# Performance work log

Measured on AMD Instinct MI355X. Metric: run time of the kernel, lower is better.

Reference implementation:

```python
import jax, jax.numpy as jnp
import numpy as np

SCALE = 10.0
THRESH = 1e-3   # nn.Threshold(eps, 0)
NORM_EPS = 1e-12  # F.normalize default eps
LEAKY_SLOPE = 0.01


def _proj(x, W1, W2):
    # x: [B, C, L]; conv1x1 == channel matmul
    h = jnp.einsum('oc,bcl->bol', W1, x)
    h = jnp.where(h >= 0, h, LEAKY_SLOPE * h)
    return jnp.einsum('oc,bcl->bol', W2, h)


def _l2norm(x):
    # normalize over channel dim (dim=1), torch F.normalize semantics
    n = jnp.sqrt(jnp.sum(x * x, axis=1, keepdims=True))
    return x / jnp.maximum(n, NORM_EPS)


def setup_inputs() -> dict:
    key = jax.random.key(0)
    k1, k2, k3, k4 = jax.random.split(key, 4)
    B, C, L, OUT = 4, 64, 4096, 64
    query = jax.random.normal(k1, (B, C, L), dtype=jnp.float32)
    kv = jax.random.normal(k2, (B, C, L), dtype=jnp.float32)
    W1 = jax.random.normal(k3, (2 * C, C), dtype=jnp.float32) * (1.0 / np.sqrt(C))
    W2 = jax.random.normal(k4, (OUT, 2 * C), dtype=jnp.float32) * (1.0 / np.sqrt(2 * C))
    return {"query": query, "key": kv, "W1": W1, "W2": W2}


def reference(query, key, W1, W2):
    # self_attention=True: query_conv is key_conv (shared weights)
    q = _l2norm(_proj(query, W1, W2))   # [B, O, L]
    k = _l2norm(_proj(key, W1, W2))     # [B, O, L]
    scores = jnp.einsum('bcl,bcm->blm', q, k) * SCALE  # [B, L, L]
    w = jax.nn.softmax(scores, axis=-1)
    return jnp.where(w > THRESH, w, 0.0)
```

## Files before the change

kernel.cpp:

```cpp
#include <hip/hip_runtime.h>
#include <math.h>

#define B 4
#define C 64
#define L 4096
#define OUTC 64
#define SCALE 10.0f
#define THRESH 1e-3f

typedef float v2f __attribute__((ext_vector_type(2)));
typedef float v4f __attribute__((ext_vector_type(4)));

__device__ __forceinline__ v2f pk_fma(v2f a, v2f b, v2f c) {
#if __has_builtin(__builtin_elementwise_fma)
    return __builtin_elementwise_fma(a, b, c);
#else
    v2f r; r.x = fmaf(a.x, b.x, c.x); r.y = fmaf(a.y, b.y, c.y); return r;
#endif
}

__global__ void __launch_bounds__(256) proj_kernel(
    const float* __restrict__ q_in, const float* __restrict__ k_in,
    const float* __restrict__ W1, const float* __restrict__ W2,
    float* __restrict__ qp, float* __restrict__ kp)
{
    int bid   = blockIdx.x;
    int which = bid >> 8;
    int b     = (bid >> 6) & 3;
    int l0    = (bid & 63) << 6;
    int t     = threadIdx.x;
    int g     = t >> 6;
    int l     = t & 63;

    const float* __restrict__ src =
        (which ? k_in : q_in) + (size_t)b * C * L + l0 + l;
    float* __restrict__ dst =
        (which ? kp : qp) + (size_t)b * OUTC * L + l0 + l;

    __shared__ float Ht[64][132];
    __shared__ float red[4][64];

    float xr[C];
    #pragma unroll
    for (int c = 0; c < C; ++c)
        xr[c] = src[(size_t)c * L];

    #pragma unroll 1
    for (int oo = 0; oo < 32; oo += 4) {
        float h4[4];
        #pragma unroll
        for (int u = 0; u < 4; ++u) {
            int o = g * 32 + oo + u;
            float h0 = 0.f, h1 = 0.f, h2 = 0.f, h3 = 0.f;
            #pragma unroll
            for (int c = 0; c < C; c += 4) {
                h0 = fmaf(W1[o * C + c + 0], xr[c + 0], h0);
                h1 = fmaf(W1[o * C + c + 1], xr[c + 1], h1);
                h2 = fmaf(W1[o * C + c + 2], xr[c + 2], h2);
                h3 = fmaf(W1[o * C + c + 3], xr[c + 3], h3);
            }
            float h = (h0 + h1) + (h2 + h3);
            h4[u] = (h >= 0.0f) ? h : 0.01f * h;
        }
        *(v4f*)&Ht[l][g * 32 + oo] = (v4f){h4[0], h4[1], h4[2], h4[3]};
    }
    __syncthreads();

    float y[16];
    #pragma unroll
    for (int u = 0; u < 16; ++u) y[u] = 0.f;

    #pragma unroll 1
    for (int hh = 0; hh < 2 * C; hh += 16) {
        float hr[16];
        #pragma unroll
        for (int r = 0; r < 16; r += 4)
            *(v4f*)&hr[r] = *(const v4f*)&Ht[l][hh + r];
        #pragma unroll
        for (int u = 0; u < 16; ++u) {
            int o = g * 16 + u;
            #pragma unroll
            for (int h = 0; h < 16; ++h)
                y[u] = fmaf(W2[o * (2 * C) + hh + h], hr[h], y[u]);
        }
    }

    float ss = 0.f;
    #pragma unroll
    for (int u = 0; u < 16; ++u) ss = fmaf(y[u], y[u], ss);
    red[g][l] = ss;
    __syncthreads();
    float tot = red[0][l] + red[1][l] + red[2][l] + red[3][l];
    float inv = 1.0f / fmaxf(sqrtf(tot), 1e-12f);

    #pragma unroll
    for (int u = 0; u < 16; ++u)
        dst[(size_t)(g * 16 + u) * L] = y[u] * inv;
}

__global__ void __launch_bounds__(512) scores_kernel(
    const float* __restrict__ qp, const float* __restrict__ kp,
    float* __restrict__ out)
{
    int bid = blockIdx.x;
    int b   = bid >> 8;
    int l0  = (bid & 255) << 4;
    int t   = threadIdx.x;

    const v4f* __restrict__ kp4 = (const v4f*)(kp + (size_t)b * C * L);
    const float* __restrict__ qb = qp + (size_t)b * C * L;

    v2f S[16][4];
    #pragma unroll
    for (int i = 0; i < 16; ++i)
        #pragma unroll
        for (int j = 0; j < 4; ++j) S[i][j] = (v2f){0.f, 0.f};

    #pragma unroll 2
    for (int c = 0; c < C; ++c) {
        v4f k0 = kp4[c * (L / 4) + t];
        v4f k1 = kp4[c * (L / 4) + t + 512];
        v2f k00 = {k0.x, k0.y}, k01 = {k0.z, k0.w};
        v2f k10 = {k1.x, k1.y}, k11 = {k1.z, k1.w};
        const float* __restrict__ qrow = qb + (size_t)c * L + l0;
        #pragma unroll
        for (int i = 0; i < 16; ++i) {
            float qi = qrow[i];
            v2f qq = {qi, qi};
            S[i][0] = pk_fma(qq, k00, S[i][0]);
            S[i][1] = pk_fma(qq, k01, S[i][1]);
            S[i][2] = pk_fma(qq, k10, S[i][2]);
            S[i][3] = pk_fma(qq, k11, S[i][3]);
        }
    }

    int wave = t >> 6, lane = t & 63;
    __shared__ float redm[16][8];
    __shared__ float reds[16][8];

    #pragma unroll
    for (int i = 0; i < 16; ++i) {
        #pragma unroll
        for (int j = 0; j < 4; ++j) S[i][j] *= (v2f){SCALE, SCALE};
        float m = fmaxf(fmaxf(fmaxf(S[i][0].x, S[i][0].y),
                              fmaxf(S[i][1].x, S[i][1].y)),
                        fmaxf(fmaxf(S[i][2].x, S[i][2].y),
                              fmaxf(S[i][3].x, S[i][3].y)));
        #pragma unroll
        for (int off = 1; off < 64; off <<= 1)
            m = fmaxf(m, __shfl_xor(m, off));
        if (lane == 0) redm[i][wave] = m;
    }
    __syncthreads();

    float rowm[16];
    #pragma unroll
    for (int i = 0; i < 16; ++i) {
        float m = redm[i][0];
        #pragma unroll
        for (int w = 1; w < 8; ++w) m = fmaxf(m, redm[i][w]);
        rowm[i] = m;
    }

    #pragma unroll
    for (int i = 0; i < 16; ++i) {
        float s = 0.f;
        #pragma unroll
        for (int j = 0; j < 4; ++j) {
            float ex = __expf(S[i][j].x - rowm[i]);
            float ey = __expf(S[i][j].y - rowm[i]);
            S[i][j] = (v2f){ex, ey};
            s += ex + ey;
        }
        #pragma unroll
        for (int off = 1; off < 64; off <<= 1)
            s += __shfl_xor(s, off);
        if (lane == 0) reds[i][wave] = s;
    }
    __syncthreads();

    v4f* __restrict__ out4 = (v4f*)out;
    #pragma unroll
    for (int i = 0; i < 16; ++i) {
        float tot = 0.f;
        #pragma unroll
        for (int w = 0; w < 8; ++w) tot += reds[i][w];
        float inv = 1.0f / tot;
        size_t rowbase = ((size_t)b * L + l0 + i) * (size_t)(L / 4);
        float w0 = S[i][0].x * inv, w1 = S[i][0].y * inv;
        float w2 = S[i][1].x * inv, w3 = S[i][1].y * inv;
        float w4 = S[i][2].x * inv, w5 = S[i][2].y * inv;
        float w6 = S[i][3].x * inv, w7 = S[i][3].y * inv;
        v4f r0 = {(w0 > THRESH) ? w0 : 0.f, (w1 > THRESH) ? w1 : 0.f,
                  (w2 > THRESH) ? w2 : 0.f, (w3 > THRESH) ? w3 : 0.f};
        v4f r1 = {(w4 > THRESH) ? w4 : 0.f, (w5 > THRESH) ? w5 : 0.f,
                  (w6 > THRESH) ? w6 : 0.f, (w7 > THRESH) ? w7 : 0.f};
        out4[rowbase + t]       = r0;
        out4[rowbase + t + 512] = r1;
    }
}

extern "C" void kernel_launch(void* const* d_in, const int* in_sizes, int n_in,
                              void* d_out, int out_size, void* d_ws, size_t ws_size,
                              hipStream_t stream) {
    const float* query = (const float*)d_in[0];
    const float* key   = (const float*)d_in[1];
    const float* W1    = (const float*)d_in[2];
    const float* W2    = (const float*)d_in[3];
    float* out = (float*)d_out;

    float* qp = (float*)d_ws;
    float* kp = qp + (size_t)B * OUTC * L;

    hipLaunchKernelGGL(proj_kernel, dim3(512), dim3(256), 0, stream,
                       query, key, W1, W2, qp, kp);
    hipLaunchKernelGGL(scores_kernel, dim3(1024), dim3(512), 0, stream,
                       qp, kp, out);
}
```

Baseline: 447.0 us.

## Halve rows per scores block, stage queries in LDS, prefetch keys, transpose proj LDS tile

```diff
diff --git a/kernel.cpp b/kernel.cpp
--- a/kernel.cpp
+++ b/kernel.cpp
@@ -37,7 +37,7 @@
     float* __restrict__ dst =
         (which ? kp : qp) + (size_t)b * OUTC * L + l0 + l;
 
-    __shared__ float Ht[64][132];
+    __shared__ float Ht[128][65];
     __shared__ float red[4][64];
 
     float xr[C];
@@ -47,7 +47,6 @@
 
     #pragma unroll 1
     for (int oo = 0; oo < 32; oo += 4) {
-        float h4[4];
         #pragma unroll
         for (int u = 0; u < 4; ++u) {
             int o = g * 32 + oo + u;
@@ -60,9 +59,8 @@
                 h3 = fmaf(W1[o * C + c + 3], xr[c + 3], h3);
             }
             float h = (h0 + h1) + (h2 + h3);
-            h4[u] = (h >= 0.0f) ? h : 0.01f * h;
-        }
-        *(v4f*)&Ht[l][g * 32 + oo] = (v4f){h4[0], h4[1], h4[2], h4[3]};
+            Ht[o][l] = (h >= 0.0f) ? h : 0.01f * h;
+        }
     }
     __syncthreads();
 
@@ -74,8 +72,8 @@
     for (int hh = 0; hh < 2 * C; hh += 16) {
         float hr[16];
         #pragma unroll
-        for (int r = 0; r < 16; r += 4)
-            *(v4f*)&hr[r] = *(const v4f*)&Ht[l][hh + r];
+        for (int r = 0; r < 16; ++r)
+            hr[r] = Ht[hh + r][l];
         #pragma unroll
         for (int u = 0; u < 16; ++u) {
             int o = g * 16 + u;
@@ -98,48 +96,63 @@
         dst[(size_t)(g * 16 + u) * L] = y[u] * inv;
 }
 
-__global__ void __launch_bounds__(512) scores_kernel(
+__global__ void __launch_bounds__(512, 4) scores_kernel(
     const float* __restrict__ qp, const float* __restrict__ kp,
     float* __restrict__ out)
 {
     int bid = blockIdx.x;
-    int b   = bid >> 8;
-    int l0  = (bid & 255) << 4;
+    int b   = bid >> 9;
+    int l0  = (bid & 511) << 3;
     int t   = threadIdx.x;
 
     const v4f* __restrict__ kp4 = (const v4f*)(kp + (size_t)b * C * L);
-    const float* __restrict__ qb = qp + (size_t)b * C * L;
-
-    v2f S[16][4];
-    #pragma unroll
-    for (int i = 0; i < 16; ++i)
+
+    __shared__ float qs[C][8];
+    {
+        int c = t >> 3, i = t & 7;
+        qs[c][i] = qp[((size_t)b * C + c) * L + l0 + i];
+    }
+    __syncthreads();
+
+    v2f S[8][4];
+    #pragma unroll
+    for (int i = 0; i < 8; ++i)
         #pragma unroll
         for (int j = 0; j < 4; ++j) S[i][j] = (v2f){0.f, 0.f};
 
-    #pragma unroll 2
+    v4f ka = kp4[t];
+    v4f kb = kp4[t + 512];
+    v4f qv = *(const v4f*)&qs[0][0];
+    v4f qw = *(const v4f*)&qs[0][4];
+
+    #pragma unroll 4
     for (int c = 0; c < C; ++c) {
-        v4f k0 = kp4[c * (L / 4) + t];
-        v4f k1 = kp4[c * (L / 4) + t + 512];
-        v2f k00 = {k0.x, k0.y}, k01 = {k0.z, k0.w};
-        v2f k10 = {k1.x, k1.y}, k11 = {k1.z, k1.w};
-        const float* __restrict__ qrow = qb + (size_t)c * L + l0;
-        #pragma unroll
-        for (int i = 0; i < 16; ++i) {
-            float qi = qrow[i];
-            v2f qq = {qi, qi};
-            S[i][0] = pk_fma(qq, k00, S[i][0]);
-            S[i][1] = pk_fma(qq, k01, S[i][1]);
-            S[i][2] = pk_fma(qq, k10, S[i][2]);
-            S[i][3] = pk_fma(qq, k11, S[i][3]);
-        }
+        int cn = (c + 1) & (C - 1);
+        v4f na = kp4[cn * (L / 4) + t];
+        v4f nb = kp4[cn * (L / 4) + t + 512];
+        v4f nqv = *(const v4f*)&qs[cn][0];
+        v4f nqw = *(const v4f*)&qs[cn][4];
+
+        v2f ka01 = {ka.x, ka.y}, ka23 = {ka.z, ka.w};
+        v2f kb01 = {kb.x, kb.y}, kb23 = {kb.z, kb.w};
+        float qarr[8] = {qv.x, qv.y, qv.z, qv.w, qw.x, qw.y, qw.z, qw.w};
+        #pragma unroll
+        for (int i = 0; i < 8; ++i) {
+            v2f qq = {qarr[i], qarr[i]};
+            S[i][0] = pk_fma(qq, ka01, S[i][0]);
+            S[i][1] = pk_fma(qq, ka23, S[i][1]);
+            S[i][2] = pk_fma(qq, kb01, S[i][2]);
+            S[i][3] = pk_fma(qq, kb23, S[i][3]);
+        }
+        ka = na; kb = nb; qv = nqv; qw = nqw;
     }
 
     int wave = t >> 6, lane = t & 63;
-    __shared__ float redm[16][8];
-    __shared__ float reds[16][8];
-
-    #pragma unroll
-    for (int i = 0; i < 16; ++i) {
+    __shared__ float redm[8][8];
+    __shared__ float reds[8][8];
+
+    #pragma unroll
+    for (int i = 0; i < 8; ++i) {
         #pragma unroll
         for (int j = 0; j < 4; ++j) S[i][j] *= (v2f){SCALE, SCALE};
         float m = fmaxf(fmaxf(fmaxf(S[i][0].x, S[i][0].y),
@@ -153,9 +166,9 @@
     }
     __syncthreads();
 
-    float rowm[16];
-    #pragma unroll
-    for (int i = 0; i < 16; ++i) {
+    float rowm[8];
+    #pragma unroll
+    for (int i = 0; i < 8; ++i) {
         float m = redm[i][0];
         #pragma unroll
         for (int w = 1; w < 8; ++w) m = fmaxf(m, redm[i][w]);
@@ -163,7 +176,7 @@
     }
 
     #pragma unroll
-    for (int i = 0; i < 16; ++i) {
+    for (int i = 0; i < 8; ++i) {
         float s = 0.f;
         #pragma unroll
         for (int j = 0; j < 4; ++j) {
@@ -181,7 +194,7 @@
 
     v4f* __restrict__ out4 = (v4f*)out;
     #pragma unroll
-    for (int i = 0; i < 16; ++i) {
+    for (int i = 0; i < 8; ++i) {
         float tot = 0.f;
         #pragma unroll
         for (int w = 0; w < 8; ++w) tot += reds[i][w];
@@ -214,6 +227,6 @@
 
     hipLaunchKernelGGL(proj_kernel, dim3(512), dim3(256), 0, stream,
                        query, key, W1, W2, qp, kp);
-    hipLaunchKernelGGL(scores_kernel, dim3(1024), dim3(512), 0, stream,
+    hipLaunchKernelGGL(scores_kernel, dim3(2048), dim3(512), 0, stream,
                        qp, kp, out);
 }
```

Result: slower. 559.1 us (+25.1%).
